# Performance work log

Measured on AMD Instinct MI355X. Metric: run time of the kernel, lower is better.

Reference implementation:

```python
import jax, jax.numpy as jnp
import numpy as np
import math

HEAD_DIM = 64

def setup_inputs() -> dict:
    key = jax.random.key(0)
    k1, k2, k3, k4 = jax.random.split(key, 4)
    B, T, E, H = 4096, 128, 256, HEAD_DIM
    x = jax.random.normal(k1, (B, T, E), dtype=jnp.float32)
    # torch nn.Linear init scale ~ U(-1/sqrt(E), 1/sqrt(E)); use scaled normal for simplicity
    s = 1.0 / math.sqrt(E)
    Wq = jax.random.normal(k2, (E, H), dtype=jnp.float32) * s
    Wk = jax.random.normal(k3, (E, H), dtype=jnp.float32) * s
    Wv = jax.random.normal(k4, (E, H), dtype=jnp.float32) * s
    return {"x": x, "Wq": Wq, "Wk": Wk, "Wv": Wv}

def reference(x, Wq, Wk, Wv):
    # x: [B, T, E]; Wq/Wk/Wv: [E, H]
    T = x.shape[1]
    H = Wq.shape[1]
    Q = jnp.einsum('bte,eh->bth', x, Wq)
    K = jnp.einsum('bte,eh->bth', x, Wk)
    V = jnp.einsum('bte,eh->bth', x, Wv)
    scores = jnp.einsum('bqh,bkh->bqk', Q, K) / jnp.sqrt(jnp.float32(H))  # [B,T,T]
    causal = jnp.tril(jnp.ones((T, T), dtype=bool))
    scores = jnp.where(causal, scores, -jnp.inf)
    weights = jax.nn.softmax(scores, axis=-1)
    # dropout omitted (eval mode / deterministic reference)
    out = jnp.einsum('bqk,bkh->bqh', weights, V)  # [B,T,H]
    return out
```

## Files before the change

kernel.cpp:

```cpp
#include <hip/hip_runtime.h>

#define NB 4096
#define TT 128
#define EE 256
#define HH 64

typedef __attribute__((ext_vector_type(8))) short bf16x8;
typedef __attribute__((ext_vector_type(4))) float f32x4;
typedef __attribute__((ext_vector_type(4))) unsigned short u16x4;

__device__ __forceinline__ unsigned short f2bf(float f) {
  union { float f; unsigned u; } c; c.f = f;
  return (unsigned short)((c.u + 0x7fffu + ((c.u >> 16) & 1u)) >> 16);
}

__device__ __forceinline__ bf16x8 cvt8(f32x4 a, f32x4 b) {
  bf16x8 r;
  r[0] = (short)f2bf(a[0]); r[1] = (short)f2bf(a[1]);
  r[2] = (short)f2bf(a[2]); r[3] = (short)f2bf(a[3]);
  r[4] = (short)f2bf(b[0]); r[5] = (short)f2bf(b[1]);
  r[6] = (short)f2bf(b[2]); r[7] = (short)f2bf(b[3]);
  return r;
}

__device__ __forceinline__ int qk_idx(int t, int h) {
  return t * 64 + ((((h >> 3) ^ t) & 7) << 3) + (h & 7);
}
__device__ __forceinline__ int p_idx(int t, int c) {
  return t * 128 + ((((c >> 3) ^ t) & 15) << 3) + (c & 7);
}
__device__ __forceinline__ int vt_idx(int h, int t) {
  return h * 128 + ((((t >> 3) ^ h) & 15) << 3) + (t & 7);
}

__global__ void prep_w(const float* __restrict__ wq, const float* __restrict__ wk,
                       const float* __restrict__ wv, unsigned short* __restrict__ wt) {
  int n = blockIdx.x;
  int e = threadIdx.x;
  const float* w = (n < 64) ? wq : (n < 128) ? wk : wv;
  wt[n * EE + e] = f2bf(w[e * HH + (n & 63)]);
}

__global__ __launch_bounds__(256, 3)
void attn_fused(const float* __restrict__ x, const unsigned short* __restrict__ wt,
                float* __restrict__ out) {
  __shared__ __align__(16) unsigned short sbuf[24576];
  unsigned short* qbuf = sbuf;
  unsigned short* kbuf = sbuf + 8192;
  unsigned short* vbuf = sbuf + 16384;
  unsigned short* pbuf = sbuf;

  const int b    = blockIdx.x;
  const int tid  = threadIdx.x;
  const int w    = tid >> 6;
  const int lane = tid & 63;
  const int quad = lane >> 4;
  const int l16  = lane & 15;
  const int m0   = 32 * w;

  const float* __restrict__ xb = x + (size_t)b * TT * EE;

  bf16x8 axf[8][2];
#pragma unroll
  for (int kc = 0; kc < 8; ++kc) {
#pragma unroll
    for (int mt = 0; mt < 2; ++mt) {
      const float* src = xb + (m0 + 16 * mt + l16) * EE + kc * 32 + quad * 8;
      f32x4 f0 = *(const f32x4*)src;
      f32x4 f1 = *(const f32x4*)(src + 4);
      axf[kc][mt] = cvt8(f0, f1);
    }
  }

#pragma unroll
  for (int pass = 0; pass < 3; ++pass) {
    f32x4 acc[4][2];
#pragma unroll
    for (int j = 0; j < 4; ++j)
#pragma unroll
      for (int mt = 0; mt < 2; ++mt)
        acc[j][mt] = (f32x4){0.f, 0.f, 0.f, 0.f};

#pragma unroll
    for (int kc = 0; kc < 8; ++kc) {
#pragma unroll
      for (int j = 0; j < 4; ++j) {
        int nt = pass * 4 + j;
        bf16x8 bfr = *(const bf16x8*)(wt + (nt * 16 + l16) * EE + kc * 32 + quad * 8);
        acc[j][0] = __builtin_amdgcn_mfma_f32_16x16x32_bf16(axf[kc][0], bfr, acc[j][0], 0, 0, 0);
        acc[j][1] = __builtin_amdgcn_mfma_f32_16x16x32_bf16(axf[kc][1], bfr, acc[j][1], 0, 0, 0);
      }
    }

#pragma unroll
    for (int j = 0; j < 4; ++j) {
      int col = j * 16 + l16;
#pragma unroll
      for (int mt = 0; mt < 2; ++mt) {
        int rbase = m0 + 16 * mt + 4 * quad;
        if (pass == 0) {
#pragma unroll
          for (int r = 0; r < 4; ++r)
            qbuf[qk_idx(rbase + r, col)] = f2bf(acc[j][mt][r]);
        } else if (pass == 1) {
#pragma unroll
          for (int r = 0; r < 4; ++r)
            kbuf[qk_idx(rbase + r, col)] = f2bf(acc[j][mt][r]);
        } else {
          u16x4 pk;
          pk[0] = f2bf(acc[j][mt][0]); pk[1] = f2bf(acc[j][mt][1]);
          pk[2] = f2bf(acc[j][mt][2]); pk[3] = f2bf(acc[j][mt][3]);
          *(u16x4*)(vbuf + vt_idx(col, rbase)) = pk;
        }
      }
    }
  }
  __syncthreads();

  const int ntS = 2 * w + 2;
  f32x4 sacc[8][2];
#pragma unroll
  for (int nt = 0; nt < 8; ++nt)
#pragma unroll
    for (int mt = 0; mt < 2; ++mt)
      sacc[nt][mt] = (f32x4){0.f, 0.f, 0.f, 0.f};

#pragma unroll
  for (int kk = 0; kk < 2; ++kk) {
    bf16x8 aq[2];
    aq[0] = *(const bf16x8*)(qbuf + qk_idx(m0 + l16, kk * 32 + quad * 8));
    aq[1] = *(const bf16x8*)(qbuf + qk_idx(m0 + 16 + l16, kk * 32 + quad * 8));
#pragma unroll
    for (int nt = 0; nt < 8; ++nt) {
      if (nt < ntS) {
        bf16x8 bk = *(const bf16x8*)(kbuf + qk_idx(nt * 16 + l16, kk * 32 + quad * 8));
        sacc[nt][0] = __builtin_amdgcn_mfma_f32_16x16x32_bf16(aq[0], bk, sacc[nt][0], 0, 0, 0);
        sacc[nt][1] = __builtin_amdgcn_mfma_f32_16x16x32_bf16(aq[1], bk, sacc[nt][1], 0, 0, 0);
      }
    }
  }
  __syncthreads();

  const float scale = 0.125f;
#pragma unroll
  for (int mt = 0; mt < 2; ++mt) {
#pragma unroll
    for (int r = 0; r < 4; ++r) {
      int row = m0 + 16 * mt + 4 * quad + r;
      float mx = -3.0e38f;
#pragma unroll
      for (int nt = 0; nt < 8; ++nt) {
        if (nt < ntS) {
          int c = nt * 16 + l16;
          float s = (c <= row) ? sacc[nt][mt][r] * scale : -3.0e38f;
          sacc[nt][mt][r] = s;
          mx = fmaxf(mx, s);
        }
      }
#pragma unroll
      for (int off = 1; off < 16; off <<= 1) mx = fmaxf(mx, __shfl_xor(mx, off, 64));
      float sum = 0.f;
#pragma unroll
      for (int nt = 0; nt < 8; ++nt) {
        if (nt < ntS) {
          float e = __expf(sacc[nt][mt][r] - mx);
          sacc[nt][mt][r] = e;
          sum += e;
        }
      }
#pragma unroll
      for (int off = 1; off < 16; off <<= 1) sum += __shfl_xor(sum, off, 64);
      float inv = 1.0f / sum;
#pragma unroll
      for (int nt = 0; nt < 8; ++nt) {
        if (nt < ntS)
          pbuf[p_idx(row, nt * 16 + l16)] = f2bf(sacc[nt][mt][r] * inv);
      }
    }
  }

  f32x4 oacc[4][2];
#pragma unroll
  for (int nt = 0; nt < 4; ++nt)
#pragma unroll
    for (int mt = 0; mt < 2; ++mt)
      oacc[nt][mt] = (f32x4){0.f, 0.f, 0.f, 0.f};

  for (int ks = 0; ks <= w; ++ks) {
    bf16x8 ap[2];
    ap[0] = *(const bf16x8*)(pbuf + p_idx(m0 + l16, ks * 32 + quad * 8));
    ap[1] = *(const bf16x8*)(pbuf + p_idx(m0 + 16 + l16, ks * 32 + quad * 8));
#pragma unroll
    for (int nt = 0; nt < 4; ++nt) {
      bf16x8 bv = *(const bf16x8*)(vbuf + vt_idx(nt * 16 + l16, ks * 32 + quad * 8));
      oacc[nt][0] = __builtin_amdgcn_mfma_f32_16x16x32_bf16(ap[0], bv, oacc[nt][0], 0, 0, 0);
      oacc[nt][1] = __builtin_amdgcn_mfma_f32_16x16x32_bf16(ap[1], bv, oacc[nt][1], 0, 0, 0);
    }
  }

  float* __restrict__ ob = out + (size_t)b * TT * HH;
#pragma unroll
  for (int mt = 0; mt < 2; ++mt) {
#pragma unroll
    for (int r = 0; r < 4; ++r) {
      int row = m0 + 16 * mt + 4 * quad + r;
#pragma unroll
      for (int nt = 0; nt < 4; ++nt)
        ob[row * HH + nt * 16 + l16] = oacc[nt][mt][r];
    }
  }
}

extern "C" void kernel_launch(void* const* d_in, const int* in_sizes, int n_in,
                              void* d_out, int out_size, void* d_ws, size_t ws_size,
                              hipStream_t stream) {
  const float* x  = (const float*)d_in[0];
  const float* wq = (const float*)d_in[1];
  const float* wk = (const float*)d_in[2];
  const float* wv = (const float*)d_in[3];
  unsigned short* wt = (unsigned short*)d_ws;
  float* outp = (float*)d_out;

  prep_w<<<dim3(192), dim3(256), 0, stream>>>(wq, wk, wv, wt);
  attn_fused<<<dim3(NB), dim3(256), 0, stream>>>(x, wt, outp);
}
```

Before: 980.3 us.

## Stream x per k-chunk with prefetch instead of holding whole bf16 tile in registers

Replaces the upfront load of the full per-wave x slab into 16 bf16x8 registers with a software-pipelined loop that converts one k-chunk at a time and prefetches the next. The projection becomes two passes: Q and K together with 8 accumulators, then V, so x is read from global memory twice instead of held in registers. Conversion now uses the packed hip bf16 intrinsics. The aim is to cut register pressure and overlap global loads with MFMA, at the cost of re-reading x for the V pass.

```diff
diff --git a/kernel.cpp b/kernel.cpp
--- a/kernel.cpp
+++ b/kernel.cpp
@@ -1,4 +1,5 @@
 #include <hip/hip_runtime.h>
+#include <hip/hip_bf16.h>
 
 #define NB 4096
 #define TT 128
@@ -14,13 +15,20 @@
   return (unsigned short)((c.u + 0x7fffu + ((c.u >> 16) & 1u)) >> 16);
 }
 
+__device__ __forceinline__ u16x4 pk4(f32x4 v) {
+  union { u16x4 s; __hip_bfloat162 h[2]; } u;
+  u.h[0] = __float22bfloat162_rn(make_float2(v[0], v[1]));
+  u.h[1] = __float22bfloat162_rn(make_float2(v[2], v[3]));
+  return u.s;
+}
+
 __device__ __forceinline__ bf16x8 cvt8(f32x4 a, f32x4 b) {
-  bf16x8 r;
-  r[0] = (short)f2bf(a[0]); r[1] = (short)f2bf(a[1]);
-  r[2] = (short)f2bf(a[2]); r[3] = (short)f2bf(a[3]);
-  r[4] = (short)f2bf(b[0]); r[5] = (short)f2bf(b[1]);
-  r[6] = (short)f2bf(b[2]); r[7] = (short)f2bf(b[3]);
-  return r;
+  union { bf16x8 v; __hip_bfloat162 h[4]; } u;
+  u.h[0] = __float22bfloat162_rn(make_float2(a[0], a[1]));
+  u.h[1] = __float22bfloat162_rn(make_float2(a[2], a[3]));
+  u.h[2] = __float22bfloat162_rn(make_float2(b[0], b[1]));
+  u.h[3] = __float22bfloat162_rn(make_float2(b[2], b[3]));
+  return u.v;
 }
 
 __device__ __forceinline__ int qk_idx(int t, int h) {
@@ -59,21 +67,71 @@
   const int m0   = 32 * w;
 
   const float* __restrict__ xb = x + (size_t)b * TT * EE;
-
-  bf16x8 axf[8][2];
-#pragma unroll
-  for (int kc = 0; kc < 8; ++kc) {
-#pragma unroll
-    for (int mt = 0; mt < 2; ++mt) {
-      const float* src = xb + (m0 + 16 * mt + l16) * EE + kc * 32 + quad * 8;
-      f32x4 f0 = *(const f32x4*)src;
-      f32x4 f1 = *(const f32x4*)(src + 4);
-      axf[kc][mt] = cvt8(f0, f1);
-    }
-  }
-
-#pragma unroll
-  for (int pass = 0; pass < 3; ++pass) {
+  const float* xrow0 = xb + (m0 + l16) * EE + quad * 8;
+  const float* xrow1 = xb + (m0 + 16 + l16) * EE + quad * 8;
+
+  {
+    f32x4 acc[8][2];
+#pragma unroll
+    for (int nt = 0; nt < 8; ++nt)
+#pragma unroll
+      for (int mt = 0; mt < 2; ++mt)
+        acc[nt][mt] = (f32x4){0.f, 0.f, 0.f, 0.f};
+
+    f32x4 nf0[4], nf1[4];
+    nf0[0] = *(const f32x4*)(xrow0);      nf0[1] = *(const f32x4*)(xrow0 + 4);
+    nf0[2] = *(const f32x4*)(xrow1);      nf0[3] = *(const f32x4*)(xrow1 + 4);
+    nf1[0] = *(const f32x4*)(xrow0 + 32); nf1[1] = *(const f32x4*)(xrow0 + 36);
+    nf1[2] = *(const f32x4*)(xrow1 + 32); nf1[3] = *(const f32x4*)(xrow1 + 36);
+
+#pragma unroll 1
+    for (int kc = 0; kc < 8; kc += 2) {
+      bf16x8 a0 = cvt8(nf0[0], nf0[1]);
+      bf16x8 a1 = cvt8(nf0[2], nf0[3]);
+      if (kc + 2 < 8) {
+        const float* p0 = xrow0 + (kc + 2) * 32;
+        const float* p1 = xrow1 + (kc + 2) * 32;
+        nf0[0] = *(const f32x4*)(p0); nf0[1] = *(const f32x4*)(p0 + 4);
+        nf0[2] = *(const f32x4*)(p1); nf0[3] = *(const f32x4*)(p1 + 4);
+      }
+#pragma unroll
+      for (int nt = 0; nt < 8; ++nt) {
+        bf16x8 bfr = *(const bf16x8*)(wt + (nt * 16 + l16) * EE + kc * 32 + quad * 8);
+        acc[nt][0] = __builtin_amdgcn_mfma_f32_16x16x32_bf16(a0, bfr, acc[nt][0], 0, 0, 0);
+        acc[nt][1] = __builtin_amdgcn_mfma_f32_16x16x32_bf16(a1, bfr, acc[nt][1], 0, 0, 0);
+      }
+      a0 = cvt8(nf1[0], nf1[1]);
+      a1 = cvt8(nf1[2], nf1[3]);
+      if (kc + 3 < 8) {
+        const float* p0 = xrow0 + (kc + 3) * 32;
+        const float* p1 = xrow1 + (kc + 3) * 32;
+        nf1[0] = *(const f32x4*)(p0); nf1[1] = *(const f32x4*)(p0 + 4);
+        nf1[2] = *(const f32x4*)(p1); nf1[3] = *(const f32x4*)(p1 + 4);
+      }
+#pragma unroll
+      for (int nt = 0; nt < 8; ++nt) {
+        bf16x8 bfr = *(const bf16x8*)(wt + (nt * 16 + l16) * EE + (kc + 1) * 32 + quad * 8);
+        acc[nt][0] = __builtin_amdgcn_mfma_f32_16x16x32_bf16(a0, bfr, acc[nt][0], 0, 0, 0);
+        acc[nt][1] = __builtin_amdgcn_mfma_f32_16x16x32_bf16(a1, bfr, acc[nt][1], 0, 0, 0);
+      }
+    }
+
+#pragma unroll
+    for (int nt = 0; nt < 8; ++nt) {
+      int col = (nt & 3) * 16 + l16;
+      unsigned short* dst = (nt < 4) ? qbuf : kbuf;
+#pragma unroll
+      for (int mt = 0; mt < 2; ++mt) {
+        int rbase = m0 + 16 * mt + 4 * quad;
+        u16x4 pv = pk4(acc[nt][mt]);
+#pragma unroll
+        for (int r = 0; r < 4; ++r)
+          dst[qk_idx(rbase + r, col)] = pv[r];
+      }
+    }
+  }
+
+  {
     f32x4 acc[4][2];
 #pragma unroll
     for (int j = 0; j < 4; ++j)
@@ -81,14 +139,41 @@
       for (int mt = 0; mt < 2; ++mt)
         acc[j][mt] = (f32x4){0.f, 0.f, 0.f, 0.f};
 
-#pragma unroll
-    for (int kc = 0; kc < 8; ++kc) {
+    f32x4 nf0[4], nf1[4];
+    nf0[0] = *(const f32x4*)(xrow0);      nf0[1] = *(const f32x4*)(xrow0 + 4);
+    nf0[2] = *(const f32x4*)(xrow1);      nf0[3] = *(const f32x4*)(xrow1 + 4);
+    nf1[0] = *(const f32x4*)(xrow0 + 32); nf1[1] = *(const f32x4*)(xrow0 + 36);
+    nf1[2] = *(const f32x4*)(xrow1 + 32); nf1[3] = *(const f32x4*)(xrow1 + 36);
+
+#pragma unroll 1
+    for (int kc = 0; kc < 8; kc += 2) {
+      bf16x8 a0 = cvt8(nf0[0], nf0[1]);
+      bf16x8 a1 = cvt8(nf0[2], nf0[3]);
+      if (kc + 2 < 8) {
+        const float* p0 = xrow0 + (kc + 2) * 32;
+        const float* p1 = xrow1 + (kc + 2) * 32;
+        nf0[0] = *(const f32x4*)(p0); nf0[1] = *(const f32x4*)(p0 + 4);
+        nf0[2] = *(const f32x4*)(p1); nf0[3] = *(const f32x4*)(p1 + 4);
+      }
 #pragma unroll
       for (int j = 0; j < 4; ++j) {
-        int nt = pass * 4 + j;
-        bf16x8 bfr = *(const bf16x8*)(wt + (nt * 16 + l16) * EE + kc * 32 + quad * 8);
-        acc[j][0] = __builtin_amdgcn_mfma_f32_16x16x32_bf16(axf[kc][0], bfr, acc[j][0], 0, 0, 0);
-        acc[j][1] = __builtin_amdgcn_mfma_f32_16x16x32_bf16(axf[kc][1], bfr, acc[j][1], 0, 0, 0);
+        bf16x8 bfr = *(const bf16x8*)(wt + ((8 + j) * 16 + l16) * EE + kc * 32 + quad * 8);
+        acc[j][0] = __builtin_amdgcn_mfma_f32_16x16x32_bf16(a0, bfr, acc[j][0], 0, 0, 0);
+        acc[j][1] = __builtin_amdgcn_mfma_f32_16x16x32_bf16(a1, bfr, acc[j][1], 0, 0, 0);
+      }
+      a0 = cvt8(nf1[0], nf1[1]);
+      a1 = cvt8(nf1[2], nf1[3]);
+      if (kc + 3 < 8) {
+        const float* p0 = xrow0 + (kc + 3) * 32;
+        const float* p1 = xrow1 + (kc + 3) * 32;
+        nf1[0] = *(const f32x4*)(p0); nf1[1] = *(const f32x4*)(p0 + 4);
+        nf1[2] = *(const f32x4*)(p1); nf1[3] = *(const f32x4*)(p1 + 4);
+      }
+#pragma unroll
+      for (int j = 0; j < 4; ++j) {
+        bf16x8 bfr = *(const bf16x8*)(wt + ((8 + j) * 16 + l16) * EE + (kc + 1) * 32 + quad * 8);
+        acc[j][0] = __builtin_amdgcn_mfma_f32_16x16x32_bf16(a0, bfr, acc[j][0], 0, 0, 0);
+        acc[j][1] = __builtin_amdgcn_mfma_f32_16x16x32_bf16(a1, bfr, acc[j][1], 0, 0, 0);
       }
     }
 
@@ -98,20 +183,7 @@
 #pragma unroll
       for (int mt = 0; mt < 2; ++mt) {
         int rbase = m0 + 16 * mt + 4 * quad;
-        if (pass == 0) {
-#pragma unroll
-          for (int r = 0; r < 4; ++r)
-            qbuf[qk_idx(rbase + r, col)] = f2bf(acc[j][mt][r]);
-        } else if (pass == 1) {
-#pragma unroll
-          for (int r = 0; r < 4; ++r)
-            kbuf[qk_idx(rbase + r, col)] = f2bf(acc[j][mt][r]);
-        } else {
-          u16x4 pk;
-          pk[0] = f2bf(acc[j][mt][0]); pk[1] = f2bf(acc[j][mt][1]);
-          pk[2] = f2bf(acc[j][mt][2]); pk[3] = f2bf(acc[j][mt][3]);
-          *(u16x4*)(vbuf + vt_idx(col, rbase)) = pk;
-        }
+        *(u16x4*)(vbuf + vt_idx(col, rbase)) = pk4(acc[j][mt]);
       }
     }
   }
```

New measurement: 1.051 ms. +7.2%, slower.
